# Kernel optimization log

Measured on AMD Instinct MI355X. Metric: run time of the kernel, lower is better.

Reference implementation:

```python
import jax, jax.numpy as jnp
import numpy as np

N_NODES = 100000

def sage_conv(x, edge_index, Wl, bl, Wr):
    # PyG SAGEConv, aggr='add', normalize=False:
    #   out = lin_l(sum_{j in N(i)} x_j) + lin_r(x_i)
    src, dst = edge_index[0], edge_index[1]
    agg = jax.ops.segment_sum(x[src], dst, num_segments=N_NODES)  # [N, F]
    return agg @ Wl.T + bl + x @ Wr.T


def setup_inputs() -> dict:
    key = jax.random.key(0)
    ks = jax.random.split(key, 7)
    F_IN, HID, C, E = 128, 256, 50, 640000
    x = jax.random.normal(ks[0], (N_NODES, F_IN), dtype=jnp.float32)
    edge_index = jax.random.randint(ks[1], (2, E), 0, N_NODES, dtype=jnp.int64)
    s1 = 1.0 / np.sqrt(F_IN)
    s2 = 1.0 / np.sqrt(HID)
    return {
        "x": x,
        "edge_index": edge_index,
        "W1l": jax.random.normal(ks[2], (HID, F_IN), dtype=jnp.float32) * s1,
        "b1l": jnp.zeros((HID,), dtype=jnp.float32),
        "W1r": jax.random.normal(ks[3], (HID, F_IN), dtype=jnp.float32) * s1,
        "W2l": jax.random.normal(ks[4], (C, HID), dtype=jnp.float32) * s2,
        "b2l": jnp.zeros((C,), dtype=jnp.float32),
        "W2r": jax.random.normal(ks[5], (C, HID), dtype=jnp.float32) * s2,
    }


def reference(x, edge_index, W1l, b1l, W1r, W2l, b2l, W2r):
    h = sage_conv(x, edge_index, W1l, b1l, W1r)
    h = jax.nn.relu(h)
    # F.dropout(p=0.5, training=False) is identity in eval mode
    out = sage_conv(h, edge_index, W2l, b2l, W2r)
    return out
```

## Files before the change

kernel.cpp:

```cpp
#include <hip/hip_runtime.h>

#define N_NODES 100000
#define MPAD    100096
#define F_IN 128
#define HID 256
#define C_OUT 50
#define N_EDGES 640000
#define CAP 32
#define NRANGE 391
#define P1BLK 256
#define EPB (N_EDGES / P1BLK)
#define CCAP 32
#define XBLK 12500

typedef __attribute__((ext_vector_type(8))) short short8;
typedef __attribute__((ext_vector_type(8))) ushort us8;
typedef __attribute__((ext_vector_type(4))) float f32x4;

struct alignas(8) us4 { ushort x, y, z, w; };

__device__ __forceinline__ ushort f2bf(float f) {
    union { float f; unsigned u; } v; v.f = f;
    unsigned r = (v.u + 0x7fffu + ((v.u >> 16) & 1u)) >> 16;
    return (ushort)r;
}

__device__ __forceinline__ float bf2f(ushort u) {
    union { unsigned u; float f; } v; v.u = ((unsigned)u) << 16;
    return v.f;
}

__device__ __forceinline__ void load_lds16(const void* gsrc, void* lds) {
    __builtin_amdgcn_global_load_lds(
        (const __attribute__((address_space(1))) void*)gsrc,
        (__attribute__((address_space(3))) void*)lds, 16, 0, 0);
}

__global__ void prep_kernel(const float* __restrict__ W1l, const float* __restrict__ W1r,
                            const float* __restrict__ W2l, const float* __restrict__ W2r,
                            ushort* __restrict__ B1t, ushort* __restrict__ B2t) {
    int idx = blockIdx.x * blockDim.x + threadIdx.x;
    if (idx < 256 * 256) {
        int o = idx >> 8, k = idx & 255;
        float v = (k < 128) ? W1l[o * 128 + k] : W1r[o * 128 + (k - 128)];
        B1t[o * 256 + k] = f2bf(v);
    }
    if (idx < 128 * 256) {
        int c = idx >> 8, k = idx & 255;
        float v = 0.f;
        if (c < C_OUT) v = W2l[c * 256 + k];
        else if (c >= 64 && c < 64 + C_OUT) v = W2r[(c - 64) * 256 + k];
        B2t[c * 256 + k] = f2bf(v);
    }
}

__global__ __launch_bounds__(256) void phase1_xcvt(const int* __restrict__ src,
                                                   const int* __restrict__ dst,
                                                   int* __restrict__ cnt1,
                                                   int* __restrict__ subbucket,
                                                   const float* __restrict__ x,
                                                   ushort* __restrict__ A1) {
    __shared__ int lcnt[NRANGE];
    int b = blockIdx.x;
    if (b < P1BLK) {
        for (int r = threadIdx.x; r < NRANGE; r += 256) lcnt[r] = 0;
        __syncthreads();
        int base = b * EPB;
        for (int i = base + (int)threadIdx.x; i < base + EPB; i += 256) {
            int d = dst[i];
            int s = src[i];
            int r = d >> 8;
            int p = atomicAdd(&lcnt[r], 1);
            if (p < CCAP) subbucket[((size_t)r * P1BLK + b) * CCAP + p] = ((d & 255) << 24) | s;
        }
        __syncthreads();
        for (int r = threadIdx.x; r < NRANGE; r += 256) cnt1[r * P1BLK + b] = lcnt[r];
    } else {
        int tid = (b - P1BLK) * 256 + threadIdx.x;
        int node = tid >> 5, q = tid & 31;
        if (node >= N_NODES) return;
        float4 v = *reinterpret_cast<const float4*>(x + (size_t)node * F_IN + q * 4);
        us4 o;
        o.x = f2bf(v.x); o.y = f2bf(v.y); o.z = f2bf(v.z); o.w = f2bf(v.w);
        *reinterpret_cast<us4*>(&A1[(size_t)node * 256 + 128 + q * 4]) = o;
    }
}

__global__ __launch_bounds__(256) void phase2_merge(const int* __restrict__ cnt1,
                                                    const int* __restrict__ subbucket,
                                                    int* __restrict__ cnt,
                                                    int* __restrict__ bucket) {
    __shared__ int lcnt2[256];
    __shared__ int lbuf[256 * CAP];
    int r = blockIdx.x, t = threadIdx.x;
    lcnt2[t] = 0;
    __syncthreads();
    int n = cnt1[r * P1BLK + t];
    if (n > CCAP) n = CCAP;
    size_t cbase = ((size_t)r * P1BLK + t) * CCAP;
    for (int k = 0; k < n; ++k) {
        unsigned u = (unsigned)subbucket[cbase + k];
        int dl = u >> 24;
        int p = atomicAdd(&lcnt2[dl], 1);
        if (p < CAP) lbuf[dl * CAP + p] = (int)(u & 0xFFFFFF);
    }
    __syncthreads();
    int node0 = r << 8;
    if (node0 + t < N_NODES) cnt[node0 + t] = lcnt2[t];
    for (int idx = t; idx < 256 * CAP; idx += 256) {
        if (node0 + (idx >> 5) < N_NODES) bucket[(size_t)node0 * CAP + idx] = lbuf[idx];
    }
}

__global__ void gather1_kernel(const int* __restrict__ cnt, const int* __restrict__ bucket,
                               ushort* __restrict__ A1) {
    int tid = blockIdx.x * blockDim.x + threadIdx.x;
    int node = tid >> 4, q = tid & 15;
    if (node >= N_NODES) return;
    int n = cnt[node];
    if (n > CAP) n = CAP;
    const int* row = bucket + (size_t)node * CAP;
    float a[8];
#pragma unroll
    for (int j = 0; j < 8; ++j) a[j] = 0.f;
    int p = 0;
    while (p + 8 <= n) {
        us8 v[8];
#pragma unroll
        for (int t = 0; t < 8; ++t) {
            int s = row[p + t];
            v[t] = *reinterpret_cast<const us8*>(&A1[(size_t)s * 256 + 128 + q * 8]);
        }
#pragma unroll
        for (int t = 0; t < 8; ++t)
#pragma unroll
            for (int j = 0; j < 8; ++j) a[j] += bf2f(v[t][j]);
        p += 8;
    }
    int rem = n - p;
    if (rem > 0) {
        us8 v[7];
#pragma unroll
        for (int t = 0; t < 7; ++t) {
            int s = (t < rem) ? row[p + t] : row[p];
            v[t] = *reinterpret_cast<const us8*>(&A1[(size_t)s * 256 + 128 + q * 8]);
        }
#pragma unroll
        for (int t = 0; t < 7; ++t) {
            if (t < rem) {
#pragma unroll
                for (int j = 0; j < 8; ++j) a[j] += bf2f(v[t][j]);
            }
        }
    }
    us8 o;
#pragma unroll
    for (int j = 0; j < 8; ++j) o[j] = f2bf(a[j]);
    *reinterpret_cast<us8*>(&A1[(size_t)node * 256 + q * 8]) = o;
}

__global__ void gather2_kernel(const ushort* __restrict__ g, const int* __restrict__ cnt,
                               const int* __restrict__ bucket, float* __restrict__ out) {
    int tid = blockIdx.x * blockDim.x + threadIdx.x;
    int node = tid >> 3, q = tid & 7;
    if (node >= N_NODES) return;
    int c = q * 8;
    if (c >= C_OUT) return;
    int n = cnt[node];
    if (n > CAP) n = CAP;
    const int* row = bucket + (size_t)node * CAP;
    float a[8];
#pragma unroll
    for (int j = 0; j < 8; ++j) a[j] = 0.f;
    int p = 0;
    while (p + 8 <= n) {
        us8 v[8];
#pragma unroll
        for (int t = 0; t < 8; ++t) {
            int s = row[p + t];
            v[t] = *reinterpret_cast<const us8*>(&g[(size_t)s * 64 + c]);
        }
#pragma unroll
        for (int t = 0; t < 8; ++t)
#pragma unroll
            for (int j = 0; j < 8; ++j) a[j] += bf2f(v[t][j]);
        p += 8;
    }
    int rem = n - p;
    if (rem > 0) {
        us8 v[7];
#pragma unroll
        for (int t = 0; t < 7; ++t) {
            int s = (t < rem) ? row[p + t] : row[p];
            v[t] = *reinterpret_cast<const us8*>(&g[(size_t)s * 64 + c]);
        }
#pragma unroll
        for (int t = 0; t < 7; ++t) {
            if (t < rem) {
#pragma unroll
                for (int j = 0; j < 8; ++j) a[j] += bf2f(v[t][j]);
            }
        }
    }
    float* po = out + (size_t)node * C_OUT;
#pragma unroll
    for (int j = 0; j < 8; ++j) {
        if (c + j < C_OUT) po[c + j] += a[j];
    }
}

__global__ __launch_bounds__(512) void gemm1_512(
    const ushort* __restrict__ A, const ushort* __restrict__ B,
    const float* __restrict__ bias, ushort* __restrict__ hOut) {
    __shared__ alignas(16) ushort As[128 * 32];
    __shared__ alignas(16) ushort Bs[256 * 32];
    const int tid = threadIdx.x;
    const int lane = tid & 63, wid = tid >> 6;
    const int wr = wid >> 2, wc = wid & 3;
    const int brow = blockIdx.x;

    f32x4 acc[4][4];
#pragma unroll
    for (int m = 0; m < 4; ++m)
#pragma unroll
        for (int n = 0; n < 4; ++n) acc[m][n] = (f32x4){0.f, 0.f, 0.f, 0.f};

    const int rA = tid >> 2,          kA = (tid & 3) * 8;
    const int cB1 = tid + 512;
    const int rB1 = cB1 >> 2,         kB1 = (cB1 & 3) * 8;
    const size_t aRow = (size_t)(brow * 128 + rA) * 256;

    const int aoffA = (lane & 15) * 32 + (lane >> 4) * 8;

    for (int kt = 0; kt < 8; ++kt) {
        const int kOff = kt * 32;
        load_lds16(A + aRow + kOff + kA, &As[tid * 8]);
        load_lds16(B + (size_t)rA * 256 + kOff + kA, &Bs[tid * 8]);
        load_lds16(B + (size_t)rB1 * 256 + kOff + kB1, &Bs[cB1 * 8]);
        __syncthreads();

        short8 af[4], bfr[4];
#pragma unroll
        for (int m = 0; m < 4; ++m)
            af[m] = *reinterpret_cast<const short8*>(&As[(wr * 64 + m * 16) * 32 + aoffA]);
#pragma unroll
        for (int n = 0; n < 4; ++n)
            bfr[n] = *reinterpret_cast<const short8*>(&Bs[(wc * 64 + n * 16) * 32 + aoffA]);
#pragma unroll
        for (int m = 0; m < 4; ++m)
#pragma unroll
            for (int n = 0; n < 4; ++n)
                acc[m][n] = __builtin_amdgcn_mfma_f32_16x16x32_bf16(af[m], bfr[n], acc[m][n], 0, 0, 0);
        __syncthreads();
    }

    const int colB = wc * 64 + (lane & 15);
    const int rowB = brow * 128 + wr * 64 + ((lane >> 4) << 2);

    float bv[4];
#pragma unroll
    for (int n = 0; n < 4; ++n) bv[n] = bias[colB + n * 16];
#pragma unroll
    for (int m = 0; m < 4; ++m) {
#pragma unroll
        for (int r = 0; r < 4; ++r) {
            int row = rowB + m * 16 + r;
            if (row >= N_NODES) continue;
#pragma unroll
            for (int n = 0; n < 4; ++n) {
                float v = acc[m][n][r] + bv[n];
                v = v > 0.f ? v : 0.f;
                hOut[(size_t)row * 256 + colB + n * 16] = f2bf(v);
            }
        }
    }
}

__global__ __launch_bounds__(256) void gemm2_kernel(
    const ushort* __restrict__ A, const ushort* __restrict__ B,
    const float* __restrict__ bias, ushort* __restrict__ gOut,
    float* __restrict__ oOut) {
    __shared__ alignas(16) ushort As[128 * 32];
    __shared__ alignas(16) ushort Bs[128 * 32];
    const int tid = threadIdx.x;
    const int lane = tid & 63, wid = tid >> 6;
    const int wr = wid >> 1, wc = wid & 1;
    const int brow = blockIdx.x;

    f32x4 acc[4][4];
#pragma unroll
    for (int m = 0; m < 4; ++m)
#pragma unroll
        for (int n = 0; n < 4; ++n) acc[m][n] = (f32x4){0.f, 0.f, 0.f, 0.f};

    const int c0 = tid, c1 = tid + 256;
    const int r0 = c0 >> 2, k80 = (c0 & 3) * 8;
    const int r1 = c1 >> 2, k81 = (c1 & 3) * 8;
    const size_t aRow0 = (size_t)(brow * 128 + r0) * 256;
    const size_t aRow1 = (size_t)(brow * 128 + r1) * 256;
    const size_t bRow0 = (size_t)r0 * 256;
    const size_t bRow1 = (size_t)r1 * 256;

    const int aoffA = (lane & 15) * 32 + (lane >> 4) * 8;

    for (int kt = 0; kt < 8; ++kt) {
        const int kOff = kt * 32;
        load_lds16(A + aRow0 + kOff + k80, &As[c0 * 8]);
        load_lds16(A + aRow1 + kOff + k81, &As[c1 * 8]);
        load_lds16(B + bRow0 + kOff + k80, &Bs[c0 * 8]);
        load_lds16(B + bRow1 + kOff + k81, &Bs[c1 * 8]);
        __syncthreads();

        short8 af[4], bfr[4];
#pragma unroll
        for (int m = 0; m < 4; ++m)
            af[m] = *reinterpret_cast<const short8*>(&As[(wr * 64 + m * 16) * 32 + aoffA]);
#pragma unroll
        for (int n = 0; n < 4; ++n)
            bfr[n] = *reinterpret_cast<const short8*>(&Bs[(wc * 64 + n * 16) * 32 + aoffA]);
#pragma unroll
        for (int m = 0; m < 4; ++m)
#pragma unroll
            for (int n = 0; n < 4; ++n)
                acc[m][n] = __builtin_amdgcn_mfma_f32_16x16x32_bf16(af[m], bfr[n], acc[m][n], 0, 0, 0);
        __syncthreads();
    }

    const int colB = wc * 64 + (lane & 15);
    const int rowB = brow * 128 + wr * 64 + ((lane >> 4) << 2);

#pragma unroll
    for (int m = 0; m < 4; ++m) {
#pragma unroll
        for (int r = 0; r < 4; ++r) {
            int row = rowB + m * 16 + r;
            if (row >= N_NODES) continue;
#pragma unroll
            for (int n = 0; n < 4; ++n) {
                int cg = colB + n * 16;
                float v = acc[m][n][r];
                if (cg < 64) {
                    gOut[(size_t)row * 64 + cg] = f2bf(v);
                } else if (cg < 64 + C_OUT) {
                    oOut[(size_t)row * C_OUT + (cg - 64)] = v + bias[cg - 64];
                }
            }
        }
    }
}

extern "C" void kernel_launch(void* const* d_in, const int* in_sizes, int n_in,
                              void* d_out, int out_size, void* d_ws, size_t ws_size,
                              hipStream_t stream) {
    const float* x   = (const float*)d_in[0];
    const int*   ei  = (const int*)d_in[1];
    const float* W1l = (const float*)d_in[2];
    const float* b1l = (const float*)d_in[3];
    const float* W1r = (const float*)d_in[4];
    const float* W2l = (const float*)d_in[5];
    const float* b2l = (const float*)d_in[6];
    const float* W2r = (const float*)d_in[7];
    float* out = (float*)d_out;

    ushort* A1    = (ushort*)d_ws;
    ushort* hbuf  = A1 + (size_t)MPAD * 256;
    ushort* B1t   = hbuf + (size_t)MPAD * 256;
    ushort* B2t   = B1t + 256 * 256;
    ushort* g     = B2t + 128 * 256;
    int* cnt      = (int*)(g + (size_t)N_NODES * 64);
    int* bucket   = cnt + N_NODES;
    int* cnt1     = bucket + (size_t)N_NODES * CAP;
    int* subbucket= cnt1 + NRANGE * P1BLK;

    const int* src = ei;
    const int* dst = ei + N_EDGES;

    prep_kernel<<<256, 256, 0, stream>>>(W1l, W1r, W2l, W2r, B1t, B2t);
    phase1_xcvt<<<P1BLK + XBLK, 256, 0, stream>>>(src, dst, cnt1, subbucket, x, A1);
    phase2_merge<<<NRANGE, 256, 0, stream>>>(cnt1, subbucket, cnt, bucket);

    gather1_kernel<<<(N_NODES * 16 + 255) / 256, 256, 0, stream>>>(cnt, bucket, A1);

    const int nbrow = MPAD / 128;
    gemm1_512<<<nbrow, 512, 0, stream>>>(A1, B1t, b1l, hbuf);
    gemm2_kernel<<<nbrow, 256, 0, stream>>>(hbuf, B2t, b2l, g, out);

    gather2_kernel<<<(N_NODES * 8 + 255) / 256, 256, 0, stream>>>(g, cnt, bucket, out);
}
```

Measured before the change: 152.1 us.

## Fuse neighbor gather into first GEMM and fold weight prep into phase1

The layer-1 neighbor aggregation now runs inside the first GEMM kernel. Each block gathers and sums its 128 nodes' neighbor features straight into LDS, then runs the first half of K from there. It then reloads the node's own bf16 features into the same LDS buffer for the second half. This removes the separate gather kernel and the global write and read of the aggregated half of A1. The weight-conversion kernel is also folded into phase1 as extra blocks, saving one launch. In exchange the GEMM blocks hold a larger LDS footprint (about 48 KB), and the MFMA work stalls behind irregular gather latency with only 782 blocks.

```diff
diff --git a/kernel.cpp b/kernel.cpp
--- a/kernel.cpp
+++ b/kernel.cpp
@@ -12,6 +12,7 @@
 #define EPB (N_EDGES / P1BLK)
 #define CCAP 32
 #define XBLK 12500
+#define WBLK 256
 
 typedef __attribute__((ext_vector_type(8))) short short8;
 typedef __attribute__((ext_vector_type(8))) ushort us8;
@@ -34,24 +35,6 @@
     __builtin_amdgcn_global_load_lds(
         (const __attribute__((address_space(1))) void*)gsrc,
         (__attribute__((address_space(3))) void*)lds, 16, 0, 0);
-}
-
-__global__ void prep_kernel(const float* __restrict__ W1l, const float* __restrict__ W1r,
-                            const float* __restrict__ W2l, const float* __restrict__ W2r,
-                            ushort* __restrict__ B1t, ushort* __restrict__ B2t) {
-    int idx = blockIdx.x * blockDim.x + threadIdx.x;
-    if (idx < 256 * 256) {
-        int o = idx >> 8, k = idx & 255;
-        float v = (k < 128) ? W1l[o * 128 + k] : W1r[o * 128 + (k - 128)];
-        B1t[o * 256 + k] = f2bf(v);
-    }
-    if (idx < 128 * 256) {
-        int c = idx >> 8, k = idx & 255;
-        float v = 0.f;
-        if (c < C_OUT) v = W2l[c * 256 + k];
-        else if (c >= 64 && c < 64 + C_OUT) v = W2r[(c - 64) * 256 + k];
-        B2t[c * 256 + k] = f2bf(v);
-    }
 }
 
 __global__ __launch_bounds__(256) void phase1_xcvt(const int* __restrict__ src,
@@ -59,7 +42,13 @@
                                                    int* __restrict__ cnt1,
                                                    int* __restrict__ subbucket,
                                                    const float* __restrict__ x,
-                                                   ushort* __restrict__ A1) {
+                                                   ushort* __restrict__ A1,
+                                                   const float* __restrict__ W1l,
+                                                   const float* __restrict__ W1r,
+                                                   const float* __restrict__ W2l,
+                                                   const float* __restrict__ W2r,
+                                                   ushort* __restrict__ B1t,
+                                                   ushort* __restrict__ B2t) {
     __shared__ int lcnt[NRANGE];
     int b = blockIdx.x;
     if (b < P1BLK) {
@@ -75,7 +64,7 @@
         }
         __syncthreads();
         for (int r = threadIdx.x; r < NRANGE; r += 256) cnt1[r * P1BLK + b] = lcnt[r];
-    } else {
+    } else if (b < P1BLK + XBLK) {
         int tid = (b - P1BLK) * 256 + threadIdx.x;
         int node = tid >> 5, q = tid & 31;
         if (node >= N_NODES) return;
@@ -83,6 +72,20 @@
         us4 o;
         o.x = f2bf(v.x); o.y = f2bf(v.y); o.z = f2bf(v.z); o.w = f2bf(v.w);
         *reinterpret_cast<us4*>(&A1[(size_t)node * 256 + 128 + q * 4]) = o;
+    } else {
+        int idx = (b - P1BLK - XBLK) * 256 + threadIdx.x;
+        if (idx < 256 * 256) {
+            int o = idx >> 8, k = idx & 255;
+            float v = (k < 128) ? W1l[o * 128 + k] : W1r[o * 128 + (k - 128)];
+            B1t[o * 256 + k] = f2bf(v);
+        }
+        if (idx < 128 * 256) {
+            int c = idx >> 8, k = idx & 255;
+            float v = 0.f;
+            if (c < C_OUT) v = W2l[c * 256 + k];
+            else if (c >= 64 && c < 64 + C_OUT) v = W2r[(c - 64) * 256 + k];
+            B2t[c * 256 + k] = f2bf(v);
+        }
     }
 }
 
@@ -112,51 +115,154 @@
     }
 }
 
-__global__ void gather1_kernel(const int* __restrict__ cnt, const int* __restrict__ bucket,
-                               ushort* __restrict__ A1) {
-    int tid = blockIdx.x * blockDim.x + threadIdx.x;
-    int node = tid >> 4, q = tid & 15;
-    if (node >= N_NODES) return;
-    int n = cnt[node];
-    if (n > CAP) n = CAP;
-    const int* row = bucket + (size_t)node * CAP;
-    float a[8];
-#pragma unroll
-    for (int j = 0; j < 8; ++j) a[j] = 0.f;
-    int p = 0;
-    while (p + 8 <= n) {
-        us8 v[8];
-#pragma unroll
-        for (int t = 0; t < 8; ++t) {
-            int s = row[p + t];
-            v[t] = *reinterpret_cast<const us8*>(&A1[(size_t)s * 256 + 128 + q * 8]);
-        }
-#pragma unroll
-        for (int t = 0; t < 8; ++t)
-#pragma unroll
-            for (int j = 0; j < 8; ++j) a[j] += bf2f(v[t][j]);
-        p += 8;
-    }
-    int rem = n - p;
-    if (rem > 0) {
-        us8 v[7];
-#pragma unroll
-        for (int t = 0; t < 7; ++t) {
-            int s = (t < rem) ? row[p + t] : row[p];
-            v[t] = *reinterpret_cast<const us8*>(&A1[(size_t)s * 256 + 128 + q * 8]);
-        }
-#pragma unroll
-        for (int t = 0; t < 7; ++t) {
-            if (t < rem) {
-#pragma unroll
-                for (int j = 0; j < 8; ++j) a[j] += bf2f(v[t][j]);
+__global__ __launch_bounds__(512) void gemm1_gather(
+    const ushort* __restrict__ A1, const int* __restrict__ cnt,
+    const int* __restrict__ bucket, const ushort* __restrict__ B,
+    const float* __restrict__ bias, ushort* __restrict__ hOut) {
+    __shared__ alignas(16) ushort As[4 * 128 * 32];
+    __shared__ alignas(16) ushort Bs[256 * 32];
+    const int tid = threadIdx.x;
+    const int lane = tid & 63, wid = tid >> 6;
+    const int wr = wid >> 2, wc = wid & 3;
+    const int brow = blockIdx.x;
+    const int aoffA = (lane & 15) * 32 + (lane >> 4) * 8;
+
+#pragma unroll
+    for (int uu = 0; uu < 4; ++uu) {
+        int u = tid + uu * 512;
+        int r = u >> 4, q = u & 15;
+        int node = brow * 128 + r;
+        float a[8];
+#pragma unroll
+        for (int j = 0; j < 8; ++j) a[j] = 0.f;
+        if (node < N_NODES) {
+            int n = cnt[node];
+            if (n > CAP) n = CAP;
+            const int* row = bucket + (size_t)node * CAP;
+            int p = 0;
+            while (p + 8 <= n) {
+                us8 v[8];
+#pragma unroll
+                for (int t = 0; t < 8; ++t) {
+                    int s = row[p + t];
+                    v[t] = *reinterpret_cast<const us8*>(&A1[(size_t)s * 256 + 128 + q * 8]);
+                }
+#pragma unroll
+                for (int t = 0; t < 8; ++t)
+#pragma unroll
+                    for (int j = 0; j < 8; ++j) a[j] += bf2f(v[t][j]);
+                p += 8;
             }
-        }
-    }
-    us8 o;
-#pragma unroll
-    for (int j = 0; j < 8; ++j) o[j] = f2bf(a[j]);
-    *reinterpret_cast<us8*>(&A1[(size_t)node * 256 + q * 8]) = o;
+            int rem = n - p;
+            if (rem > 0) {
+                us8 v[7];
+#pragma unroll
+                for (int t = 0; t < 7; ++t) {
+                    int s = (t < rem) ? row[p + t] : row[p];
+                    v[t] = *reinterpret_cast<const us8*>(&A1[(size_t)s * 256 + 128 + q * 8]);
+                }
+#pragma unroll
+                for (int t = 0; t < 7; ++t) {
+                    if (t < rem) {
+#pragma unroll
+                        for (int j = 0; j < 8; ++j) a[j] += bf2f(v[t][j]);
+                    }
+                }
+            }
+        }
+        us8 o;
+#pragma unroll
+        for (int j = 0; j < 8; ++j) o[j] = f2bf(a[j]);
+        *reinterpret_cast<us8*>(&As[(q >> 2) * 4096 + r * 32 + (q & 3) * 8]) = o;
+    }
+    __syncthreads();
+
+    f32x4 acc[4][4];
+#pragma unroll
+    for (int m = 0; m < 4; ++m)
+#pragma unroll
+        for (int n = 0; n < 4; ++n) acc[m][n] = (f32x4){0.f, 0.f, 0.f, 0.f};
+
+    const int rB0 = tid >> 2, kB0 = (tid & 3) * 8;
+    const int cB1 = tid + 512;
+    const int rB1 = cB1 >> 2, kB1 = (cB1 & 3) * 8;
+
+    for (int kt = 0; kt < 4; ++kt) {
+        const int kOff = kt * 32;
+        load_lds16(B + (size_t)rB0 * 256 + kOff + kB0, &Bs[tid * 8]);
+        load_lds16(B + (size_t)rB1 * 256 + kOff + kB1, &Bs[cB1 * 8]);
+        __syncthreads();
+        short8 af[4], bfr[4];
+#pragma unroll
+        for (int m = 0; m < 4; ++m)
+            af[m] = *reinterpret_cast<const short8*>(&As[kt * 4096 + (wr * 64 + m * 16) * 32 + aoffA]);
+#pragma unroll
+        for (int n = 0; n < 4; ++n)
+            bfr[n] = *reinterpret_cast<const short8*>(&Bs[(wc * 64 + n * 16) * 32 + aoffA]);
+#pragma unroll
+        for (int m = 0; m < 4; ++m)
+#pragma unroll
+            for (int n = 0; n < 4; ++n)
+                acc[m][n] = __builtin_amdgcn_mfma_f32_16x16x32_bf16(af[m], bfr[n], acc[m][n], 0, 0, 0);
+        __syncthreads();
+    }
+
+#pragma unroll
+    for (int uu = 0; uu < 4; ++uu) {
+        int u = tid + uu * 512;
+        int r = u >> 4, q = u & 15;
+        int node = brow * 128 + r;
+        us8 xv;
+        if (node < N_NODES) {
+            xv = *reinterpret_cast<const us8*>(&A1[(size_t)node * 256 + 128 + q * 8]);
+        } else {
+#pragma unroll
+            for (int j = 0; j < 8; ++j) xv[j] = 0;
+        }
+        *reinterpret_cast<us8*>(&As[(q >> 2) * 4096 + r * 32 + (q & 3) * 8]) = xv;
+    }
+    __syncthreads();
+
+    for (int kt = 4; kt < 8; ++kt) {
+        const int kOff = kt * 32;
+        load_lds16(B + (size_t)rB0 * 256 + kOff + kB0, &Bs[tid * 8]);
+        load_lds16(B + (size_t)rB1 * 256 + kOff + kB1, &Bs[cB1 * 8]);
+        __syncthreads();
+        short8 af[4], bfr[4];
+#pragma unroll
+        for (int m = 0; m < 4; ++m)
+            af[m] = *reinterpret_cast<const short8*>(&As[(kt - 4) * 4096 + (wr * 64 + m * 16) * 32 + aoffA]);
+#pragma unroll
+        for (int n = 0; n < 4; ++n)
+            bfr[n] = *reinterpret_cast<const short8*>(&Bs[(wc * 64 + n * 16) * 32 + aoffA]);
+#pragma unroll
+        for (int m = 0; m < 4; ++m)
+#pragma unroll
+            for (int n = 0; n < 4; ++n)
+                acc[m][n] = __builtin_amdgcn_mfma_f32_16x16x32_bf16(af[m], bfr[n], acc[m][n], 0, 0, 0);
+        __syncthreads();
+    }
+
+    const int colB = wc * 64 + (lane & 15);
+    const int rowB = brow * 128 + wr * 64 + ((lane >> 4) << 2);
+
+    float bv[4];
+#pragma unroll
+    for (int n = 0; n < 4; ++n) bv[n] = bias[colB + n * 16];
+#pragma unroll
+    for (int m = 0; m < 4; ++m) {
+#pragma unroll
+        for (int r = 0; r < 4; ++r) {
+            int row = rowB + m * 16 + r;
+            if (row >= N_NODES) continue;
+#pragma unroll
+            for (int n = 0; n < 4; ++n) {
+                float v = acc[m][n][r] + bv[n];
+                v = v > 0.f ? v : 0.f;
+                hOut[(size_t)row * 256 + colB + n * 16] = f2bf(v);
+            }
+        }
+    }
 }
 
 __global__ void gather2_kernel(const ushort* __restrict__ g, const int* __restrict__ cnt,
@@ -206,73 +312,6 @@
 #pragma unroll
     for (int j = 0; j < 8; ++j) {
         if (c + j < C_OUT) po[c + j] += a[j];
-    }
-}
-
-__global__ __launch_bounds__(512) void gemm1_512(
-    const ushort* __restrict__ A, const ushort* __restrict__ B,
-    const float* __restrict__ bias, ushort* __restrict__ hOut) {
-    __shared__ alignas(16) ushort As[128 * 32];
-    __shared__ alignas(16) ushort Bs[256 * 32];
-    const int tid = threadIdx.x;
-    const int lane = tid & 63, wid = tid >> 6;
-    const int wr = wid >> 2, wc = wid & 3;
-    const int brow = blockIdx.x;
-
-    f32x4 acc[4][4];
-#pragma unroll
-    for (int m = 0; m < 4; ++m)
-#pragma unroll
-        for (int n = 0; n < 4; ++n) acc[m][n] = (f32x4){0.f, 0.f, 0.f, 0.f};
-
-    const int rA = tid >> 2,          kA = (tid & 3) * 8;
-    const int cB1 = tid + 512;
-    const int rB1 = cB1 >> 2,         kB1 = (cB1 & 3) * 8;
-    const size_t aRow = (size_t)(brow * 128 + rA) * 256;
-
-    const int aoffA = (lane & 15) * 32 + (lane >> 4) * 8;
-
-    for (int kt = 0; kt < 8; ++kt) {
-        const int kOff = kt * 32;
-        load_lds16(A + aRow + kOff + kA, &As[tid * 8]);
-        load_lds16(B + (size_t)rA * 256 + kOff + kA, &Bs[tid * 8]);
-        load_lds16(B + (size_t)rB1 * 256 + kOff + kB1, &Bs[cB1 * 8]);
-        __syncthreads();
-
-        short8 af[4], bfr[4];
-#pragma unroll
-        for (int m = 0; m < 4; ++m)
-            af[m] = *reinterpret_cast<const short8*>(&As[(wr * 64 + m * 16) * 32 + aoffA]);
-#pragma unroll
-        for (int n = 0; n < 4; ++n)
-            bfr[n] = *reinterpret_cast<const short8*>(&Bs[(wc * 64 + n * 16) * 32 + aoffA]);
-#pragma unroll
-        for (int m = 0; m < 4; ++m)
-#pragma unroll
-            for (int n = 0; n < 4; ++n)
-                acc[m][n] = __builtin_amdgcn_mfma_f32_16x16x32_bf16(af[m], bfr[n], acc[m][n], 0, 0, 0);
-        __syncthreads();
-    }
-
-    const int colB = wc * 64 + (lane & 15);
-    const int rowB = brow * 128 + wr * 64 + ((lane >> 4) << 2);
-
-    float bv[4];
-#pragma unroll
-    for (int n = 0; n < 4; ++n) bv[n] = bias[colB + n * 16];
-#pragma unroll
-    for (int m = 0; m < 4; ++m) {
-#pragma unroll
-        for (int r = 0; r < 4; ++r) {
-            int row = rowB + m * 16 + r;
-            if (row >= N_NODES) continue;
-#pragma unroll
-            for (int n = 0; n < 4; ++n) {
-                float v = acc[m][n][r] + bv[n];
-                v = v > 0.f ? v : 0.f;
-                hOut[(size_t)row * 256 + colB + n * 16] = f2bf(v);
-            }
-        }
     }
 }
 
@@ -375,14 +414,12 @@
     const int* src = ei;
     const int* dst = ei + N_EDGES;
 
-    prep_kernel<<<256, 256, 0, stream>>>(W1l, W1r, W2l, W2r, B1t, B2t);
-    phase1_xcvt<<<P1BLK + XBLK, 256, 0, stream>>>(src, dst, cnt1, subbucket, x, A1);
+    phase1_xcvt<<<P1BLK + XBLK + WBLK, 256, 0, stream>>>(
+        src, dst, cnt1, subbucket, x, A1, W1l, W1r, W2l, W2r, B1t, B2t);
     phase2_merge<<<NRANGE, 256, 0, stream>>>(cnt1, subbucket, cnt, bucket);
 
-    gather1_kernel<<<(N_NODES * 16 + 255) / 256, 256, 0, stream>>>(cnt, bucket, A1);
-
     const int nbrow = MPAD / 128;
-    gemm1_512<<<nbrow, 512, 0, stream>>>(A1, B1t, b1l, hbuf);
+    gemm1_gather<<<nbrow, 512, 0, stream>>>(A1, cnt, bucket, B1t, b1l, hbuf);
     gemm2_kernel<<<nbrow, 256, 0, stream>>>(hbuf, B2t, b2l, g, out);
 
     gather2_kernel<<<(N_NODES * 8 + 255) / 256, 256, 0, stream>>>(g, cnt, bucket, out);
```

After: 174.4 us. 1.15x slower.
